# Kernel tuning notes

Hardware: AMD Instinct MI355X
Metric: run time of the kernel (lower is better)

## Reference

```python
import jax, jax.numpy as jnp
import numpy as np

B, S, K, N, NO = 2, 4096, 4096, 4096, 32


def setup_inputs() -> dict:
    key = jax.random.key(0)
    k0, k1, k2, k3 = jax.random.split(key, 4)
    # activations with a few high-magnitude 'outlier' columns (LLM.int8-style)
    x = jax.random.normal(k0, (B, S, K), dtype=jnp.float16)
    ind = jnp.sort(jax.random.randint(k1, (NO,), 0, K)).astype(jnp.int32)
    x = x.at[:, :, ind].multiply(jnp.float16(30.0))
    # fp16 master weight -> quantize exactly as the module's init path does
    w = (jax.random.normal(k2, (N, K), dtype=jnp.float32) * 0.02)
    weight_cache = w[:, ind].astype(jnp.float16)          # original outlier cols
    w_z = w.at[:, ind].set(0.0)                            # zero outlier cols
    scale = (jnp.max(jnp.abs(w_z), axis=1) / 127.0)        # per-out-channel scale
    q_weight = jnp.clip(jnp.round(w_z / scale[:, None]), -128.0, 127.0).astype(jnp.int8)
    bias = (jax.random.normal(k3, (N,), dtype=jnp.float32) * 0.01)
    # packed (N, 2): [:, 0] = dequant scale, [:, 1] = bias (matches q_scale_col layout)
    scale_col = jnp.stack([scale, bias], axis=1).astype(jnp.float16)
    return {
        "x": x,
        "q_weight": q_weight,
        "scale_col": scale_col,
        "weight_cache": weight_cache,
        "ind": ind,
    }


def reference(x, q_weight, scale_col, weight_cache, ind):
    # mixgemmforward_dynamic: per-row dynamic activation quant, int8 GEMM,
    # per-(row,col) dequant, fused bias add, fp16 outlier-column correction.
    Bx, Sx, Kx = x.shape
    Nx = q_weight.shape[0]
    xf = x.astype(jnp.float32).reshape(-1, Kx)                    # [M, K]
    scale_row = jnp.max(jnp.abs(xf), axis=1, keepdims=True) / 127.0  # [M, 1]
    q_x = jnp.round(jnp.clip(xf / scale_row, -128.0, 127.0))      # int-valued f32
    acc = q_x @ q_weight.astype(jnp.float32).T                    # [M, N] int GEMM
    w_scale = scale_col[:, 0].astype(jnp.float32)                 # [N]
    bias = scale_col[:, 1].astype(jnp.float32)                    # [N]
    y = acc * scale_row * w_scale[None, :] + bias[None, :]
    # outlier correction: fp16 GEMM over the extracted outlier columns
    y = y + xf[:, ind] @ weight_cache.astype(jnp.float32).T
    return y.reshape(Bx, Sx, Nx).astype(jnp.float16)
```

## Files before the change

kernel.cpp:

```cpp
#include <hip/hip_runtime.h>
#include <stdint.h>


typedef float    f32x4  __attribute__((ext_vector_type(4)));
typedef int      i32x4  __attribute__((ext_vector_type(4)));
typedef _Float16 half8  __attribute__((ext_vector_type(8)));
typedef _Float16 half4  __attribute__((ext_vector_type(4)));

#define MTOT 8192
#define NTOT 4096
#define KTOT 4096

__global__ __launch_bounds__(256) void pack_kernel(
    const int* __restrict__ qw32, int8_t* __restrict__ qw8,
    const float* __restrict__ wc, _Float16* __restrict__ wch)
{
  const int bid = blockIdx.x;
  if (bid < 4096) {
    const int base = (bid * 256 + threadIdx.x) * 16;
    const i32x4* p = (const i32x4*)(qw32 + base);
    uint32_t o[4];
#pragma unroll
    for (int g = 0; g < 4; ++g) {
      const i32x4 v = p[g];
      o[g] = (uint32_t)(v[0] & 255) | ((uint32_t)(v[1] & 255) << 8) |
             ((uint32_t)(v[2] & 255) << 16) | ((uint32_t)(v[3] & 255) << 24);
    }
    *(i32x4*)(qw8 + base) = i32x4{(int)o[0], (int)o[1], (int)o[2], (int)o[3]};
  } else {
    const int idx = ((bid - 4096) * 256 + threadIdx.x) * 4;
    const float4 v = *(const float4*)(wc + idx);
    half4 h = {(_Float16)v.x, (_Float16)v.y, (_Float16)v.z, (_Float16)v.w};
    *(half4*)(wch + idx) = h;
  }
}

__global__ __launch_bounds__(256) void quant_kernel(
    const float* __restrict__ x, const int* __restrict__ ind,
    int8_t* __restrict__ qx, float* __restrict__ srow, _Float16* __restrict__ xo)
{
  const int row = blockIdx.x;
  const int t = threadIdx.x;
  const float* xrow = x + (size_t)row * KTOT;
  const float4* xr = (const float4*)xrow;
  float4 v[4];
#pragma unroll
  for (int g = 0; g < 4; ++g) v[g] = xr[4 * t + g];

  float am = 0.f;
#pragma unroll
  for (int g = 0; g < 4; ++g) {
    am = fmaxf(am, fmaxf(fmaxf(fabsf(v[g].x), fabsf(v[g].y)),
                         fmaxf(fabsf(v[g].z), fabsf(v[g].w))));
  }
#pragma unroll
  for (int off = 32; off; off >>= 1)
    am = fmaxf(am, __shfl_xor(am, off, 64));
  __shared__ float red[4];
  if ((t & 63) == 0) red[t >> 6] = am;
  __syncthreads();
  am = fmaxf(fmaxf(red[0], red[1]), fmaxf(red[2], red[3]));

  const float rscale = 127.0f / am;

  uint32_t o[4];
#pragma unroll
  for (int g = 0; g < 4; ++g) {
    const float4 w = v[g];
    const int q0 = (int)rintf(fminf(fmaxf(w.x * rscale, -128.f), 127.f));
    const int q1 = (int)rintf(fminf(fmaxf(w.y * rscale, -128.f), 127.f));
    const int q2 = (int)rintf(fminf(fmaxf(w.z * rscale, -128.f), 127.f));
    const int q3 = (int)rintf(fminf(fmaxf(w.w * rscale, -128.f), 127.f));
    o[g] = (uint32_t)(q0 & 255) | ((uint32_t)(q1 & 255) << 8) |
           ((uint32_t)(q2 & 255) << 16) | ((uint32_t)(q3 & 255) << 24);
  }
  *(i32x4*)(qx + (size_t)row * KTOT + 16 * t) =
      i32x4{(int)o[0], (int)o[1], (int)o[2], (int)o[3]};

  if (t < 32) xo[row * 32 + t] = (_Float16)xrow[ind[t]];
  if (t == 0) srow[row] = am / 127.0f;
}

__global__ __launch_bounds__(256) void mixgemm_kernel(
    const int8_t* __restrict__ qx, const int8_t* __restrict__ qw,
    const float* __restrict__ srow, const float* __restrict__ sc,
    const _Float16* __restrict__ xo, const _Float16* __restrict__ wc,
    float* __restrict__ out)
{
  __shared__ int8_t lA[128 * 64];
  __shared__ int8_t lB[128 * 64];

  const int t = threadIdx.x;
  const int lane = t & 63;
  const int wid = t >> 6;
  const int wm = wid >> 1, wn = wid & 1;
  const int bx = blockIdx.x;
  const int tn = bx & 31;
  const int tm = bx >> 5;
  const int bm0 = tm * 128, bn0 = tn * 128;

  const int idx0 = t, idx1 = t + 256;
  const int r0 = idx0 >> 2, c0 = idx0 & 3;
  const int r1 = idx1 >> 2, c1 = idx1 & 3;
  const int w0 = r0 * 64 + ((c0 ^ (r0 & 3)) * 16);
  const int w1 = r1 * 64 + ((c1 ^ (r1 & 3)) * 16);
  const int8_t* gA0 = qx + (size_t)(bm0 + r0) * KTOT + c0 * 16;
  const int8_t* gA1 = qx + (size_t)(bm0 + r1) * KTOT + c1 * 16;
  const int8_t* gB0 = qw + (size_t)(bn0 + r0) * KTOT + c0 * 16;
  const int8_t* gB1 = qw + (size_t)(bn0 + r1) * KTOT + c1 * 16;

  int roA[4], roB[4];
#pragma unroll
  for (int i = 0; i < 4; ++i) {
    const int ra = wm * 64 + i * 16 + (lane & 15);
    roA[i] = ra * 64 + (((lane >> 4) ^ (ra & 3)) * 16);
    const int rb = wn * 64 + i * 16 + (lane & 15);
    roB[i] = rb * 64 + (((lane >> 4) ^ (rb & 3)) * 16);
  }

  i32x4 acc[4][4];
#pragma unroll
  for (int i = 0; i < 4; ++i)
#pragma unroll
    for (int j = 0; j < 4; ++j) acc[i][j] = i32x4{0, 0, 0, 0};

  for (int kt = 0; kt < KTOT; kt += 64) {
    const i32x4 sa0 = *(const i32x4*)(gA0 + kt);
    const i32x4 sa1 = *(const i32x4*)(gA1 + kt);
    const i32x4 sb0 = *(const i32x4*)(gB0 + kt);
    const i32x4 sb1 = *(const i32x4*)(gB1 + kt);
    __syncthreads();
    *(i32x4*)(lA + w0) = sa0;
    *(i32x4*)(lA + w1) = sa1;
    *(i32x4*)(lB + w0) = sb0;
    *(i32x4*)(lB + w1) = sb1;
    __syncthreads();
    i32x4 af[4], bfr[4];
#pragma unroll
    for (int i = 0; i < 4; ++i) {
      af[i]  = *(const i32x4*)(lA + roA[i]);
      bfr[i] = *(const i32x4*)(lB + roB[i]);
    }
#pragma unroll
    for (int i = 0; i < 4; ++i)
#pragma unroll
      for (int j = 0; j < 4; ++j)
        acc[i][j] = __builtin_amdgcn_mfma_i32_16x16x64_i8(af[i], bfr[j], acc[i][j], 0, 0, 0);
  }

  {
    const char* xob = (const char*)xo + (size_t)bm0 * 64;
    const char* wcb = (const char*)wc + (size_t)bn0 * 64;
    const i32x4 xs0 = *(const i32x4*)(xob + idx0 * 16);
    const i32x4 xs1 = *(const i32x4*)(xob + idx1 * 16);
    const i32x4 ws0 = *(const i32x4*)(wcb + idx0 * 16);
    const i32x4 ws1 = *(const i32x4*)(wcb + idx1 * 16);
    __syncthreads();
    *(i32x4*)(lA + w0) = xs0;
    *(i32x4*)(lA + w1) = xs1;
    *(i32x4*)(lB + w0) = ws0;
    *(i32x4*)(lB + w1) = ws1;
    __syncthreads();
  }
  f32x4 corr[4][4];
#pragma unroll
  for (int i = 0; i < 4; ++i)
#pragma unroll
    for (int j = 0; j < 4; ++j) corr[i][j] = f32x4{0.f, 0.f, 0.f, 0.f};
  {
    half8 xf[4], wf[4];
#pragma unroll
    for (int i = 0; i < 4; ++i) {
      xf[i] = __builtin_bit_cast(half8, *(const i32x4*)(lA + roA[i]));
      wf[i] = __builtin_bit_cast(half8, *(const i32x4*)(lB + roB[i]));
    }
#pragma unroll
    for (int i = 0; i < 4; ++i)
#pragma unroll
      for (int j = 0; j < 4; ++j)
        corr[i][j] = __builtin_amdgcn_mfma_f32_16x16x32_f16(xf[i], wf[j], corr[i][j], 0, 0, 0);
  }

#pragma unroll
  for (int i = 0; i < 4; ++i) {
    const int rowg = bm0 + wm * 64 + i * 16 + (lane >> 4) * 4;
    const f32x4 sr = *(const f32x4*)(srow + rowg);
#pragma unroll
    for (int j = 0; j < 4; ++j) {
      const int colg = bn0 + wn * 64 + j * 16 + (lane & 15);
      const float2 scb = ((const float2*)sc)[colg];
      float* op = out + (size_t)rowg * NTOT + colg;
#pragma unroll
      for (int r = 0; r < 4; ++r) {
        const float y = (float)acc[i][j][r] * (sr[r] * scb.x) + scb.y + corr[i][j][r];
        op[(size_t)r * NTOT] = y;
      }
    }
  }
}

extern "C" void kernel_launch(void* const* d_in, const int* in_sizes, int n_in,
                              void* d_out, int out_size, void* d_ws, size_t ws_size,
                              hipStream_t stream) {
  (void)in_sizes; (void)n_in; (void)out_size; (void)ws_size;
  const float* x    = (const float*)d_in[0];
  const int*   qw32 = (const int*)d_in[1];
  const float* sc   = (const float*)d_in[2];
  const float* wcf  = (const float*)d_in[3];
  const int*   ind  = (const int*)d_in[4];
  float* out = (float*)d_out;

  char* ws = (char*)d_ws;
  int8_t*   qx   = (int8_t*)ws;
  float*    srow = (float*)(ws + 33554432);
  _Float16* xo   = (_Float16*)(ws + 33587200);
  int8_t*   qw8  = (int8_t*)(ws + 34111488);
  _Float16* wch  = (_Float16*)(ws + 50888704);

  pack_kernel<<<4096 + 128, 256, 0, stream>>>(qw32, qw8, wcf, wch);
  quant_kernel<<<MTOT, 256, 0, stream>>>(x, ind, qx, srow, xo);
  mixgemm_kernel<<<(MTOT / 128) * (NTOT / 128), 256, 0, stream>>>(qx, qw8, srow, sc, xo, wch, out);
}
```

Before: 465.1 us.

## Use direct global-to-LDS loads, swizzle block order, and restructure pack/quant kernels

The GEMM main loop now uses global_load_lds to move A/B tiles straight into shared memory instead of staging them through registers. A new XOR swizzle keyed on row>>1 keeps the LDS layout conflict-free under that load pattern. Workgroup indices are remapped so that consecutive blocks are spread across tile rows, which may change L2 reuse. The quant kernel now handles one row per wavefront, removing the block-level reduction and barrier, and the pack kernel's accesses are made coalesced per iteration.

```diff
diff --git a/kernel.cpp b/kernel.cpp
--- a/kernel.cpp
+++ b/kernel.cpp
@@ -10,25 +10,33 @@
 #define MTOT 8192
 #define NTOT 4096
 #define KTOT 4096
+
+#define SWZ(r) (((r) >> 1) & 3)
+
+static __device__ __forceinline__ void gload16(const int8_t* g, int8_t* l) {
+  __builtin_amdgcn_global_load_lds(
+      (const __attribute__((address_space(1))) void*)g,
+      (__attribute__((address_space(3))) void*)l, 16, 0, 0);
+}
 
 __global__ __launch_bounds__(256) void pack_kernel(
     const int* __restrict__ qw32, int8_t* __restrict__ qw8,
     const float* __restrict__ wc, _Float16* __restrict__ wch)
 {
   const int bid = blockIdx.x;
+  const int t = threadIdx.x;
   if (bid < 4096) {
-    const int base = (bid * 256 + threadIdx.x) * 16;
-    const i32x4* p = (const i32x4*)(qw32 + base);
-    uint32_t o[4];
+    const int base = bid * 4096;
 #pragma unroll
     for (int g = 0; g < 4; ++g) {
-      const i32x4 v = p[g];
-      o[g] = (uint32_t)(v[0] & 255) | ((uint32_t)(v[1] & 255) << 8) |
-             ((uint32_t)(v[2] & 255) << 16) | ((uint32_t)(v[3] & 255) << 24);
-    }
-    *(i32x4*)(qw8 + base) = i32x4{(int)o[0], (int)o[1], (int)o[2], (int)o[3]};
+      const int off = g * 1024 + t * 4;
+      const i32x4 v = *(const i32x4*)(qw32 + base + off);
+      const uint32_t o = (uint32_t)(v[0] & 255) | ((uint32_t)(v[1] & 255) << 8) |
+                         ((uint32_t)(v[2] & 255) << 16) | ((uint32_t)(v[3] & 255) << 24);
+      *(uint32_t*)(qw8 + base + off) = o;
+    }
   } else {
-    const int idx = ((bid - 4096) * 256 + threadIdx.x) * 4;
+    const int idx = (bid - 4096) * 1024 + t * 4;
     const float4 v = *(const float4*)(wc + idx);
     half4 h = {(_Float16)v.x, (_Float16)v.y, (_Float16)v.z, (_Float16)v.w};
     *(half4*)(wch + idx) = h;
@@ -39,46 +47,39 @@
     const float* __restrict__ x, const int* __restrict__ ind,
     int8_t* __restrict__ qx, float* __restrict__ srow, _Float16* __restrict__ xo)
 {
-  const int row = blockIdx.x;
   const int t = threadIdx.x;
+  const int w = t >> 6, l = t & 63;
+  const int row = blockIdx.x * 4 + w;
   const float* xrow = x + (size_t)row * KTOT;
   const float4* xr = (const float4*)xrow;
-  float4 v[4];
-#pragma unroll
-  for (int g = 0; g < 4; ++g) v[g] = xr[4 * t + g];
+
+  float4 v[16];
+#pragma unroll
+  for (int g = 0; g < 16; ++g) v[g] = xr[g * 64 + l];
 
   float am = 0.f;
 #pragma unroll
-  for (int g = 0; g < 4; ++g) {
+  for (int g = 0; g < 16; ++g)
     am = fmaxf(am, fmaxf(fmaxf(fabsf(v[g].x), fabsf(v[g].y)),
                          fmaxf(fabsf(v[g].z), fabsf(v[g].w))));
-  }
 #pragma unroll
   for (int off = 32; off; off >>= 1)
     am = fmaxf(am, __shfl_xor(am, off, 64));
-  __shared__ float red[4];
-  if ((t & 63) == 0) red[t >> 6] = am;
-  __syncthreads();
-  am = fmaxf(fmaxf(red[0], red[1]), fmaxf(red[2], red[3]));
 
   const float rscale = 127.0f / am;
-
-  uint32_t o[4];
-#pragma unroll
-  for (int g = 0; g < 4; ++g) {
-    const float4 w = v[g];
-    const int q0 = (int)rintf(fminf(fmaxf(w.x * rscale, -128.f), 127.f));
-    const int q1 = (int)rintf(fminf(fmaxf(w.y * rscale, -128.f), 127.f));
-    const int q2 = (int)rintf(fminf(fmaxf(w.z * rscale, -128.f), 127.f));
-    const int q3 = (int)rintf(fminf(fmaxf(w.w * rscale, -128.f), 127.f));
-    o[g] = (uint32_t)(q0 & 255) | ((uint32_t)(q1 & 255) << 8) |
-           ((uint32_t)(q2 & 255) << 16) | ((uint32_t)(q3 & 255) << 24);
-  }
-  *(i32x4*)(qx + (size_t)row * KTOT + 16 * t) =
-      i32x4{(int)o[0], (int)o[1], (int)o[2], (int)o[3]};
-
-  if (t < 32) xo[row * 32 + t] = (_Float16)xrow[ind[t]];
-  if (t == 0) srow[row] = am / 127.0f;
+  uint32_t* qrow = (uint32_t*)(qx + (size_t)row * KTOT);
+#pragma unroll
+  for (int g = 0; g < 16; ++g) {
+    const float4 u = v[g];
+    const int q0 = (int)rintf(fminf(fmaxf(u.x * rscale, -128.f), 127.f));
+    const int q1 = (int)rintf(fminf(fmaxf(u.y * rscale, -128.f), 127.f));
+    const int q2 = (int)rintf(fminf(fmaxf(u.z * rscale, -128.f), 127.f));
+    const int q3 = (int)rintf(fminf(fmaxf(u.w * rscale, -128.f), 127.f));
+    qrow[g * 64 + l] = (uint32_t)(q0 & 255) | ((uint32_t)(q1 & 255) << 8) |
+                       ((uint32_t)(q2 & 255) << 16) | ((uint32_t)(q3 & 255) << 24);
+  }
+  if (l < 32) xo[row * 32 + l] = (_Float16)xrow[ind[l]];
+  if (l == 0) srow[row] = am / 127.0f;
 }
 
 __global__ __launch_bounds__(256) void mixgemm_kernel(
@@ -94,28 +95,27 @@
   const int lane = t & 63;
   const int wid = t >> 6;
   const int wm = wid >> 1, wn = wid & 1;
-  const int bx = blockIdx.x;
-  const int tn = bx & 31;
-  const int tm = bx >> 5;
+
+  const int bid = blockIdx.x;
+  const int swz = (bid & 7) * 256 + (bid >> 3);
+  const int tn = swz & 31;
+  const int tm = swz >> 5;
   const int bm0 = tm * 128, bn0 = tn * 128;
 
-  const int idx0 = t, idx1 = t + 256;
-  const int r0 = idx0 >> 2, c0 = idx0 & 3;
-  const int r1 = idx1 >> 2, c1 = idx1 & 3;
-  const int w0 = r0 * 64 + ((c0 ^ (r0 & 3)) * 16);
-  const int w1 = r1 * 64 + ((c1 ^ (r1 & 3)) * 16);
-  const int8_t* gA0 = qx + (size_t)(bm0 + r0) * KTOT + c0 * 16;
-  const int8_t* gA1 = qx + (size_t)(bm0 + r1) * KTOT + c1 * 16;
-  const int8_t* gB0 = qw + (size_t)(bn0 + r0) * KTOT + c0 * 16;
-  const int8_t* gB1 = qw + (size_t)(bn0 + r1) * KTOT + c1 * 16;
+  const int rst = wid * 32 + (lane >> 2);
+  const int cst = ((lane & 3) ^ SWZ(rst)) * 16;
+  const int8_t* gA0 = qx + (size_t)(bm0 + rst) * KTOT + cst;
+  const int8_t* gB0 = qw + (size_t)(bn0 + rst) * KTOT + cst;
+  int8_t* dA = lA + wid * 2048;
+  int8_t* dB = lB + wid * 2048;
 
   int roA[4], roB[4];
 #pragma unroll
   for (int i = 0; i < 4; ++i) {
     const int ra = wm * 64 + i * 16 + (lane & 15);
-    roA[i] = ra * 64 + (((lane >> 4) ^ (ra & 3)) * 16);
+    roA[i] = ra * 64 + (((lane >> 4) ^ SWZ(ra)) * 16);
     const int rb = wn * 64 + i * 16 + (lane & 15);
-    roB[i] = rb * 64 + (((lane >> 4) ^ (rb & 3)) * 16);
+    roB[i] = rb * 64 + (((lane >> 4) ^ SWZ(rb)) * 16);
   }
 
   i32x4 acc[4][4];
@@ -125,15 +125,11 @@
     for (int j = 0; j < 4; ++j) acc[i][j] = i32x4{0, 0, 0, 0};
 
   for (int kt = 0; kt < KTOT; kt += 64) {
-    const i32x4 sa0 = *(const i32x4*)(gA0 + kt);
-    const i32x4 sa1 = *(const i32x4*)(gA1 + kt);
-    const i32x4 sb0 = *(const i32x4*)(gB0 + kt);
-    const i32x4 sb1 = *(const i32x4*)(gB1 + kt);
-    __syncthreads();
-    *(i32x4*)(lA + w0) = sa0;
-    *(i32x4*)(lA + w1) = sa1;
-    *(i32x4*)(lB + w0) = sb0;
-    *(i32x4*)(lB + w1) = sb1;
+    __syncthreads();
+    gload16(gA0 + kt, dA);
+    gload16(gA0 + kt + 16 * KTOT, dA + 1024);
+    gload16(gB0 + kt, dB);
+    gload16(gB0 + kt + 16 * KTOT, dB + 1024);
     __syncthreads();
     i32x4 af[4], bfr[4];
 #pragma unroll
@@ -149,6 +145,11 @@
   }
 
   {
+    const int idx0 = t, idx1 = t + 256;
+    const int r0 = idx0 >> 2, c0 = idx0 & 3;
+    const int r1 = idx1 >> 2, c1 = idx1 & 3;
+    const int w0 = r0 * 64 + ((c0 ^ SWZ(r0)) * 16);
+    const int w1 = r1 * 64 + ((c1 ^ SWZ(r1)) * 16);
     const char* xob = (const char*)xo + (size_t)bm0 * 64;
     const char* wcb = (const char*)wc + (size_t)bn0 * 64;
     const i32x4 xs0 = *(const i32x4*)(xob + idx0 * 16);
@@ -218,6 +219,6 @@
   _Float16* wch  = (_Float16*)(ws + 50888704);
 
   pack_kernel<<<4096 + 128, 256, 0, stream>>>(qw32, qw8, wcf, wch);
-  quant_kernel<<<MTOT, 256, 0, stream>>>(x, ind, qx, srow, xo);
+  quant_kernel<<<MTOT / 4, 256, 0, stream>>>(x, ind, qx, srow, xo);
   mixgemm_kernel<<<(MTOT / 128) * (NTOT / 128), 256, 0, stream>>>(qx, qw8, srow, sc, xo, wch, out);
 }
```

After: 446.9 us. 3.9% less time.
